# Kernel tuning notes

Measured on AMD Instinct MI355X. Metric: run time of the kernel, lower is better.

## Reference

```python
import jax, jax.numpy as jnp
import numpy as np

B, S, P, N = 256, 128, 100, 500
E, H, L, F = 256, 4, 2, 1024   # embed, heads, layers, ffn
V, U, I = 50000, 10000, 10000


def setup_inputs() -> dict:
    key = jax.random.key(0)
    ks = jax.random.split(key, 32)
    u = lambda k, shp: jax.random.uniform(k, shp, jnp.float32, -0.1, 0.1)
    n = lambda k, shp, s=0.02: jax.random.normal(k, shp, jnp.float32) * s
    inp = {
        'attr': jax.random.randint(ks[0], (B, S), 0, V),
        'attr_inds': jax.random.randint(ks[1], (B, S), 0, S),
        'attr_tf': jax.random.uniform(ks[2], (B, S), jnp.float32),
        'attr_feat': jax.random.normal(ks[3], (B, 13), jnp.float32),
        'attr_lens': jax.random.randint(ks[4], (B,), S // 2, S + 1).at[0].set(S),
        'attr_lens_user': jax.random.randint(ks[5], (B,), 0, S),
        'attr_lens_item': jax.random.randint(ks[6], (B,), 0, S),
        'user_ids': jax.random.randint(ks[7], (B,), 0, U),
        'item_ids': jax.random.randint(ks[8], (B,), 0, I),
        'pos_targets': jax.random.randint(ks[9], (B, P), 0, V),
        'pos_lens': jax.random.randint(ks[10], (B,), 1, P + 1).at[0].set(P),
        'neg_targets': jax.random.randint(ks[11], (B, N), 0, V),
        'neg_lens': jax.random.randint(ks[12], (B,), 1, N + 1).at[0].set(N),
        # parameters (init_uniform(-0.1,0.1) like f_init_weight)
        'attr_emb': u(ks[13], (V, E)),
        'user_emb': u(ks[14], (U, E)),
        'item_emb': u(ks[15], (I, E)),
        'out_emb': u(ks[16], (V, 3 * E)),
        'fw_W': n(ks[17], (1, 13), 0.1),
        'fw_b': jnp.zeros((1,), jnp.float32),
        'qkv_w': n(ks[18], (L, 3 * E, E)),
        'qkv_b': jnp.zeros((L, 3 * E), jnp.float32),
        'attn_out_w': n(ks[19], (L, E, E)),
        'attn_out_b': jnp.zeros((L, E), jnp.float32),
        'ln1_s': jnp.ones((L, E), jnp.float32),
        'ln1_b': jnp.zeros((L, E), jnp.float32),
        'ff1_w': n(ks[20], (L, F, E)),
        'ff1_b': jnp.zeros((L, F), jnp.float32),
        'ff2_w': n(ks[21], (L, E, F)),
        'ff2_b': jnp.zeros((L, E), jnp.float32),
        'ln2_s': jnp.ones((L, E), jnp.float32),
        'ln2_b': jnp.zeros((L, E), jnp.float32),
    }
    return inp


def _ln(x, s, b, eps=1e-5):
    m = jnp.mean(x, axis=-1, keepdims=True)
    v = jnp.mean(jnp.square(x - m), axis=-1, keepdims=True)
    return (x - m) * jax.lax.rsqrt(v + eps) * s + b


def _encoder_layer(x, pad, p):
    # PyTorch TransformerEncoderLayer (post-norm, relu, dropout=0/eval)
    b, s, e = x.shape
    hd = e // H
    qkv = x @ p['qkv_w'].T + p['qkv_b']                      # [B,S,3E]
    q, k, v = jnp.split(qkv, 3, axis=-1)
    q = q.reshape(b, s, H, hd)
    k = k.reshape(b, s, H, hd)
    v = v.reshape(b, s, H, hd)
    scores = jnp.einsum('bqhd,bkhd->bhqk', q, k) / jnp.sqrt(jnp.float32(hd))
    scores = scores + jnp.where(pad[:, None, None, :], -1e9, 0.0)
    a = jax.nn.softmax(scores, axis=-1)
    o = jnp.einsum('bhqk,bkhd->bqhd', a, v).reshape(b, s, e)
    o = o @ p['attn_out_w'].T + p['attn_out_b']
    x = _ln(x + o, p['ln1_s'], p['ln1_b'])
    h = jax.nn.relu(x @ p['ff1_w'].T + p['ff1_b'])
    h = h @ p['ff2_w'].T + p['ff2_b']
    return _ln(x + h, p['ln2_s'], p['ln2_b'])


def reference(attr, attr_inds, attr_tf, attr_feat, attr_lens, attr_lens_user,
              attr_lens_item, user_ids, item_ids, pos_targets, pos_lens,
              neg_targets, neg_lens, attr_emb, user_emb, item_emb, out_emb,
              fw_W, fw_b, qkv_w, qkv_b, attn_out_w, attn_out_b, ln1_s, ln1_b,
              ff1_w, ff1_b, ff2_w, ff2_b, ln2_s, ln2_b):
    b, s = attr.shape
    pos = jnp.arange(s)
    pad = pos[None, :] >= attr_lens[:, None]                 # True = padding
    x = attr_emb[attr]                                       # [B,S,E]
    for l in range(qkv_w.shape[0]):
        p = {'qkv_w': qkv_w[l], 'qkv_b': qkv_b[l],
             'attn_out_w': attn_out_w[l], 'attn_out_b': attn_out_b[l],
             'ln1_s': ln1_s[l], 'ln1_b': ln1_b[l],
             'ff1_w': ff1_w[l], 'ff1_b': ff1_b[l],
             'ff2_w': ff2_w[l], 'ff2_b': ff2_b[l],
             'ln2_s': ln2_s[l], 'ln2_b': ln2_b[l]}
        x = _encoder_layer(x, pad, p)
    # per-sample scalar user weight; vectorized ragged user/item tf weighting
    w_user = jax.nn.sigmoid(attr_feat @ fw_W.T + fw_b)[:, 0]           # [B]
    side = jnp.where(pos[None, :] < attr_lens_user[:, None],
                     w_user[:, None], 1.0 - w_user[:, None])           # [B,S]
    weight = attr_tf * side * (~pad)                                   # [B,S]
    attr_x = jnp.einsum('bs,bse->be', weight, x)                       # [B,E]
    output = jnp.concatenate([user_emb[user_ids], attr_x,
                              item_emb[item_ids]], axis=-1)            # [B,3E]
    pos_logits = jnp.einsum('bpe,be->bp', out_emb[pos_targets], output)
    neg_logits = jnp.einsum('bne,be->bn', out_emb[neg_targets], output)
    pos_valid = jnp.arange(pos_targets.shape[1])[None, :] < pos_lens[:, None]
    neg_valid = jnp.arange(neg_targets.shape[1])[None, :] < neg_lens[:, None]
    logits = jnp.concatenate([pos_logits, neg_logits], axis=-1)
    mask = jnp.concatenate([pos_valid, neg_valid], axis=-1)
    new_targets = jnp.concatenate([jnp.ones_like(pos_targets),
                                   jnp.zeros_like(neg_targets)], axis=1)
    new_targets = new_targets * mask.astype(new_targets.dtype)
    return logits, mask, new_targets
```

## Files before the change

kernel.cpp:

```cpp
#include <hip/hip_runtime.h>
#include <hip/hip_bf16.h>

typedef __bf16 bf16_t;
typedef __bf16 bf16x8 __attribute__((ext_vector_type(8)));
typedef __bf16 bf16x4 __attribute__((ext_vector_type(4)));
typedef float f32x4 __attribute__((ext_vector_type(4)));

#define B_ 256
#define S_ 128
#define E_ 256
#define H_ 4
#define HD_ 64
#define F_ 1024
#define TPOS_ 100
#define TNEG_ 500
#define TT_ 600
#define ROWS_ (B_ * S_)

__global__ __launch_bounds__(256) void cvtall_kernel(
        const float* __restrict__ sq, const float* __restrict__ sa,
        const float* __restrict__ s1, const float* __restrict__ s2,
        bf16_t* __restrict__ dq, bf16_t* __restrict__ da,
        bf16_t* __restrict__ d1, bf16_t* __restrict__ d2) {
    int i = blockIdx.x * 256 + threadIdx.x;
    if (i < 393216) { dq[i] = (bf16_t)sq[i]; }
    else if (i < 524288) { int j = i - 393216; da[j] = (bf16_t)sa[j]; }
    else if (i < 1048576) { int j = i - 524288; d1[j] = (bf16_t)s1[j]; }
    else { int j = i - 1048576; d2[j] = (bf16_t)s2[j]; }
}

__global__ __launch_bounds__(256) void embed_kernel(const int* __restrict__ attr,
        const float* __restrict__ emb, bf16_t* __restrict__ xb) {
    int row = blockIdx.x * 4 + (threadIdx.x >> 6);
    int lane = threadIdx.x & 63;
    int idx = attr[row];
    float4 v = reinterpret_cast<const float4*>(emb + (size_t)idx * E_)[lane];
    bf16x4 o; o[0] = (bf16_t)v.x; o[1] = (bf16_t)v.y; o[2] = (bf16_t)v.z; o[3] = (bf16_t)v.w;
    *reinterpret_cast<bf16x4*>(xb + (size_t)row * E_ + lane * 4) = o;
}

template<bool RELU>
__global__ __launch_bounds__(256) void gemm_kernel(
        const bf16_t* __restrict__ A, const bf16_t* __restrict__ W,
        const float* __restrict__ bias, bf16_t* __restrict__ outB, int M, int N, int K) {
    __shared__ bf16_t lA[2][128 * 32];
    __shared__ bf16_t lB[2][128 * 32];
    int tid = threadIdx.x;
    int wave = tid >> 6, lane = tid & 63;
    int wr = wave >> 1, wc = wave & 1;
    int mBase = blockIdx.y * 128;
    int nBase = blockIdx.x * 128;
    int r16 = lane & 15, kg = lane >> 4;

    int srow = wave * 16 + (lane >> 2);
    int scol = (lane & 3) * 8;
    const bf16_t* gA = A + (size_t)(mBase + srow) * K + scol;
    const bf16_t* gB = W + (size_t)(nBase + srow) * K + scol;
    int ldst = wave * 512;

    f32x4 acc[4][4] = {};

    #define STAGE(buf, k0) { \
        _Pragma("unroll") \
        for (int iss = 0; iss < 2; iss++) { \
            __builtin_amdgcn_global_load_lds( \
                (const __attribute__((address_space(1))) void*)(gA + (size_t)iss * 64 * K + (k0)), \
                (__attribute__((address_space(3))) void*)(&lA[buf][iss * 2048 + ldst]), 16, 0, 0); \
            __builtin_amdgcn_global_load_lds( \
                (const __attribute__((address_space(1))) void*)(gB + (size_t)iss * 64 * K + (k0)), \
                (__attribute__((address_space(3))) void*)(&lB[buf][iss * 2048 + ldst]), 16, 0, 0); \
        } }

    STAGE(0, 0);
    int cur = 0;
    for (int k0 = 0; k0 < K; k0 += 32) {
        __syncthreads();
        if (k0 + 32 < K) STAGE(cur ^ 1, k0 + 32);
        bf16x8 a[4], b[4];
        #pragma unroll
        for (int i = 0; i < 4; i++) {
            a[i] = *reinterpret_cast<const bf16x8*>(&lA[cur][(wr * 64 + i * 16 + r16) * 32 + kg * 8]);
            b[i] = *reinterpret_cast<const bf16x8*>(&lB[cur][(wc * 64 + i * 16 + r16) * 32 + kg * 8]);
        }
        #pragma unroll
        for (int mi = 0; mi < 4; mi++)
            #pragma unroll
            for (int ni = 0; ni < 4; ni++)
                acc[mi][ni] = __builtin_amdgcn_mfma_f32_16x16x32_bf16(a[mi], b[ni], acc[mi][ni], 0, 0, 0);
        cur ^= 1;
    }
    #undef STAGE

    #pragma unroll
    for (int mi = 0; mi < 4; mi++) {
        #pragma unroll
        for (int ni = 0; ni < 4; ni++) {
            int col = nBase + wc * 64 + ni * 16 + r16;
            float bv = bias[col];
            #pragma unroll
            for (int j = 0; j < 4; j++) {
                int row = mBase + wr * 64 + mi * 16 + kg * 4 + j;
                float v = acc[mi][ni][j] + bv;
                if (RELU) v = v > 0.f ? v : 0.f;
                outB[(size_t)row * N + col] = (bf16_t)v;
            }
        }
    }
}

__global__ __launch_bounds__(256) void gemm_ln_kernel(
        const bf16_t* __restrict__ A, const bf16_t* __restrict__ W,
        const float* __restrict__ bias, const float* __restrict__ sc,
        const float* __restrict__ bi, bf16_t* __restrict__ xb, int M, int K) {
    __shared__ bf16_t lA[2][64 * 32];
    __shared__ bf16_t lB[2][256 * 32];
    __shared__ float psum[64][2][2];
    int tid = threadIdx.x;
    int wave = tid >> 6, lane = tid & 63;
    int wm = wave >> 1, wn = wave & 1;
    int mBase = blockIdx.x * 64;
    int r16 = lane & 15, kg = lane >> 4;

    const bf16_t* gA = A + (size_t)(mBase + wave * 16 + (lane >> 2)) * K + (lane & 3) * 8;
    const bf16_t* gB = W + (size_t)((lane >> 2)) * K + (lane & 3) * 8;

    f32x4 acc[2][8] = {};

    #define STAGE2(buf, k0) { \
        __builtin_amdgcn_global_load_lds( \
            (const __attribute__((address_space(1))) void*)(gA + (k0)), \
            (__attribute__((address_space(3))) void*)(&lA[buf][wave * 512]), 16, 0, 0); \
        _Pragma("unroll") \
        for (int iss = 0; iss < 4; iss++) { \
            int q = wave * 4 + iss; \
            __builtin_amdgcn_global_load_lds( \
                (const __attribute__((address_space(1))) void*)(gB + (size_t)q * 16 * K + (k0)), \
                (__attribute__((address_space(3))) void*)(&lB[buf][q * 512]), 16, 0, 0); \
        } }

    STAGE2(0, 0);
    int cur = 0;
    for (int k0 = 0; k0 < K; k0 += 32) {
        __syncthreads();
        if (k0 + 32 < K) STAGE2(cur ^ 1, k0 + 32);
        bf16x8 a[2], b[8];
        #pragma unroll
        for (int mi = 0; mi < 2; mi++)
            a[mi] = *reinterpret_cast<const bf16x8*>(&lA[cur][(wm * 32 + mi * 16 + r16) * 32 + kg * 8]);
        #pragma unroll
        for (int ni = 0; ni < 8; ni++)
            b[ni] = *reinterpret_cast<const bf16x8*>(&lB[cur][(wn * 128 + ni * 16 + r16) * 32 + kg * 8]);
        #pragma unroll
        for (int mi = 0; mi < 2; mi++)
            #pragma unroll
            for (int ni = 0; ni < 8; ni++)
                acc[mi][ni] = __builtin_amdgcn_mfma_f32_16x16x32_bf16(a[mi], b[ni], acc[mi][ni], 0, 0, 0);
        cur ^= 1;
    }
    #undef STAGE2

    float bv[8];
    #pragma unroll
    for (int ni = 0; ni < 8; ni++) bv[ni] = bias[wn * 128 + ni * 16 + r16];
    #pragma unroll
    for (int mi = 0; mi < 2; mi++) {
        #pragma unroll
        for (int j = 0; j < 4; j++) {
            int rl = wm * 32 + mi * 16 + kg * 4 + j;
            const bf16_t* rrow = xb + (size_t)(mBase + rl) * 256;
            float s = 0.f, q = 0.f;
            #pragma unroll
            for (int ni = 0; ni < 8; ni++) {
                int col = wn * 128 + ni * 16 + r16;
                float v = acc[mi][ni][j] + bv[ni] + (float)rrow[col];
                acc[mi][ni][j] = v;
                s += v; q += v * v;
            }
            #pragma unroll
            for (int m = 1; m < 16; m <<= 1) { s += __shfl_xor(s, m); q += __shfl_xor(q, m); }
            if (r16 == 0) { psum[rl][wn][0] = s; psum[rl][wn][1] = q; }
        }
    }
    __syncthreads();
    #pragma unroll
    for (int mi = 0; mi < 2; mi++) {
        #pragma unroll
        for (int j = 0; j < 4; j++) {
            int rl = wm * 32 + mi * 16 + kg * 4 + j;
            float s = psum[rl][0][0] + psum[rl][1][0];
            float qq = psum[rl][0][1] + psum[rl][1][1];
            float mean = s * (1.0f / 256.0f);
            float var = qq * (1.0f / 256.0f) - mean * mean;
            float inv = rsqrtf(var + 1e-5f);
            bf16_t* orow = xb + (size_t)(mBase + rl) * 256;
            #pragma unroll
            for (int ni = 0; ni < 8; ni++) {
                int col = wn * 128 + ni * 16 + r16;
                float o = (acc[mi][ni][j] - mean) * inv * sc[col] + bi[col];
                orow[col] = (bf16_t)o;
            }
        }
    }
}

__global__ __launch_bounds__(256) void attn_kernel(const bf16_t* __restrict__ qkv,
        const int* __restrict__ lens, bf16_t* __restrict__ out) {
    __shared__ bf16_t p[S_][S_ + 8];
    __shared__ bf16_t vl[HD_][S_ + 8];
    int bh = blockIdx.x; int b = bh >> 2, h = bh & 3;
    int wave = threadIdx.x >> 6, lane = threadIdx.x & 63;
    int r16 = lane & 15, kg = lane >> 4;
    int q0 = wave * 32;
    int len = lens[b];
    const bf16_t* qbase = qkv + (size_t)b * S_ * 768;

    {
        int sl = (wave & 1) * 64 + lane;
        const bf16_t* vsrc = qbase + (size_t)sl * 768 + 512 + h * HD_;
        #pragma unroll
        for (int pass = 0; pass < 4; pass++) {
            int d0 = (pass * 2 + (wave >> 1)) * 8;
            bf16x8 v = *reinterpret_cast<const bf16x8*>(vsrc + d0);
            #pragma unroll
            for (int j = 0; j < 8; j++) vl[d0 + j][sl] = v[j];
        }
    }

    f32x4 acc[2][8] = {};
    #pragma unroll
    for (int ks = 0; ks < 2; ks++) {
        int kOff = h * HD_ + ks * 32 + kg * 8;
        bf16x8 a[2], bb[8];
        #pragma unroll
        for (int mi = 0; mi < 2; mi++)
            a[mi] = *reinterpret_cast<const bf16x8*>(qbase + (size_t)(q0 + mi * 16 + r16) * 768 + kOff);
        #pragma unroll
        for (int ni = 0; ni < 8; ni++)
            bb[ni] = *reinterpret_cast<const bf16x8*>(qbase + (size_t)(ni * 16 + r16) * 768 + 256 + kOff);
        #pragma unroll
        for (int mi = 0; mi < 2; mi++)
            #pragma unroll
            for (int ni = 0; ni < 8; ni++)
                acc[mi][ni] = __builtin_amdgcn_mfma_f32_16x16x32_bf16(a[mi], bb[ni], acc[mi][ni], 0, 0, 0);
    }
    #pragma unroll
    for (int mi = 0; mi < 2; mi++) {
        #pragma unroll
        for (int j = 0; j < 4; j++) {
            float vals[8]; float mx = -1e30f;
            #pragma unroll
            for (int ni = 0; ni < 8; ni++) {
                int kp = ni * 16 + r16;
                float v = acc[mi][ni][j] * 0.125f;
                vals[ni] = (kp < len) ? v : -1e30f;
                mx = fmaxf(mx, vals[ni]);
            }
            #pragma unroll
            for (int m = 1; m < 16; m <<= 1) mx = fmaxf(mx, __shfl_xor(mx, m));
            float sum = 0.f;
            #pragma unroll
            for (int ni = 0; ni < 8; ni++) {
                vals[ni] = (vals[ni] > -1e29f) ? __expf(vals[ni] - mx) : 0.f;
                sum += vals[ni];
            }
            #pragma unroll
            for (int m = 1; m < 16; m <<= 1) sum += __shfl_xor(sum, m);
            float inv = 1.0f / sum;
            int row = q0 + mi * 16 + kg * 4 + j;
            #pragma unroll
            for (int ni = 0; ni < 8; ni++)
                p[row][ni * 16 + r16] = (bf16_t)(vals[ni] * inv);
        }
    }
    __syncthreads();
    f32x4 acc2[2][4] = {};
    #pragma unroll
    for (int ks = 0; ks < 4; ks++) {
        int k = ks * 32 + kg * 8;
        bf16x8 a[2], bb[4];
        #pragma unroll
        for (int mi = 0; mi < 2; mi++)
            a[mi] = *reinterpret_cast<const bf16x8*>(&p[q0 + mi * 16 + r16][k]);
        #pragma unroll
        for (int ni = 0; ni < 4; ni++)
            bb[ni] = *reinterpret_cast<const bf16x8*>(&vl[ni * 16 + r16][k]);
        #pragma unroll
        for (int mi = 0; mi < 2; mi++)
            #pragma unroll
            for (int ni = 0; ni < 4; ni++)
                acc2[mi][ni] = __builtin_amdgcn_mfma_f32_16x16x32_bf16(a[mi], bb[ni], acc2[mi][ni], 0, 0, 0);
    }
    #pragma unroll
    for (int mi = 0; mi < 2; mi++)
        #pragma unroll
        for (int ni = 0; ni < 4; ni++)
            #pragma unroll
            for (int j = 0; j < 4; j++) {
                int q = q0 + mi * 16 + kg * 4 + j;
                int d = ni * 16 + r16;
                out[((size_t)b * S_ + q) * E_ + h * HD_ + d] = (bf16_t)acc2[mi][ni][j];
            }
}

__global__ void wuser_kernel(const float* __restrict__ feat, const float* __restrict__ W,
                             const float* __restrict__ bb, float* __restrict__ wu) {
    int b = threadIdx.x;
    if (b < B_) {
        float z = bb[0];
        #pragma unroll
        for (int i = 0; i < 13; i++) z += feat[b * 13 + i] * W[i];
        wu[b] = 1.f / (1.f + __expf(-z));
    }
}

__global__ __launch_bounds__(256) void pool_kernel(
        const bf16_t* __restrict__ xb, const float* __restrict__ attr_tf,
        const int* __restrict__ lens, const int* __restrict__ lens_user,
        const float* __restrict__ wu, const int* __restrict__ uid, const int* __restrict__ iid,
        const float* __restrict__ user_emb, const float* __restrict__ item_emb,
        float* __restrict__ outvec) {
    int b = blockIdx.x, t = threadIdx.x;
    __shared__ float wrow[S_];
    if (t < S_) {
        float w = (t < lens[b]) ? attr_tf[b * S_ + t] : 0.f;
        float side = (t < lens_user[b]) ? wu[b] : (1.f - wu[b]);
        wrow[t] = w * side;
    }
    __syncthreads();
    float acc = 0.f;
    const bf16_t* xr = xb + (size_t)b * S_ * E_ + t;
    #pragma unroll 4
    for (int s = 0; s < S_; s++) acc += wrow[s] * (float)xr[(size_t)s * E_];
    outvec[b * 768 + 256 + t] = acc;
    outvec[b * 768 + t] = user_emb[(size_t)uid[b] * E_ + t];
    outvec[b * 768 + 512 + t] = item_emb[(size_t)iid[b] * E_ + t];
}

__global__ __launch_bounds__(256) void logits_kernel(
        const float* __restrict__ outvec, const float* __restrict__ out_emb,
        const int* __restrict__ pos_t, const int* __restrict__ pos_l,
        const int* __restrict__ neg_t, const int* __restrict__ neg_l,
        float* __restrict__ dout) {
    int g = blockIdx.x * 4 + (threadIdx.x >> 6);
    int lane = threadIdx.x & 63;
    int b = g / TT_, t = g - b * TT_;
    int tgt, valid, ispos;
    if (t < TPOS_) { tgt = pos_t[b * TPOS_ + t]; valid = (t < pos_l[b]); ispos = 1; }
    else { int tn = t - TPOS_; tgt = neg_t[b * TNEG_ + tn]; valid = (tn < neg_l[b]); ispos = 0; }
    const float4* e4 = reinterpret_cast<const float4*>(out_emb + (size_t)tgt * 768);
    const float4* o4 = reinterpret_cast<const float4*>(outvec + (size_t)b * 768);
    float acc = 0.f;
    #pragma unroll
    for (int c = 0; c < 3; c++) {
        float4 a = e4[c * 64 + lane];
        float4 o = o4[c * 64 + lane];
        acc += a.x * o.x + a.y * o.y + a.z * o.z + a.w * o.w;
    }
    #pragma unroll
    for (int m = 1; m < 64; m <<= 1) acc += __shfl_xor(acc, m);
    if (lane == 0) {
        size_t i = (size_t)b * TT_ + t;
        dout[i] = acc;
        dout[(size_t)B_ * TT_ + i] = valid ? 1.0f : 0.0f;
        dout[2 * (size_t)B_ * TT_ + i] = (valid && ispos) ? 1.0f : 0.0f;
    }
}

extern "C" void kernel_launch(void* const* d_in, const int* in_sizes, int n_in,
                              void* d_out, int out_size, void* d_ws, size_t ws_size,
                              hipStream_t stream) {
    const int*   attr        = (const int*)d_in[0];
    const float* attr_tf     = (const float*)d_in[2];
    const float* attr_feat   = (const float*)d_in[3];
    const int*   attr_lens   = (const int*)d_in[4];
    const int*   attr_lens_u = (const int*)d_in[5];
    const int*   user_ids    = (const int*)d_in[7];
    const int*   item_ids    = (const int*)d_in[8];
    const int*   pos_targets = (const int*)d_in[9];
    const int*   pos_lens    = (const int*)d_in[10];
    const int*   neg_targets = (const int*)d_in[11];
    const int*   neg_lens    = (const int*)d_in[12];
    const float* attr_emb    = (const float*)d_in[13];
    const float* user_emb    = (const float*)d_in[14];
    const float* item_emb    = (const float*)d_in[15];
    const float* out_emb     = (const float*)d_in[16];
    const float* fw_W        = (const float*)d_in[17];
    const float* fw_b        = (const float*)d_in[18];
    const float* qkv_w       = (const float*)d_in[19];
    const float* qkv_b       = (const float*)d_in[20];
    const float* attn_out_w  = (const float*)d_in[21];
    const float* attn_out_b  = (const float*)d_in[22];
    const float* ln1_s       = (const float*)d_in[23];
    const float* ln1_b       = (const float*)d_in[24];
    const float* ff1_w       = (const float*)d_in[25];
    const float* ff1_b       = (const float*)d_in[26];
    const float* ff2_w       = (const float*)d_in[27];
    const float* ff2_b       = (const float*)d_in[28];
    const float* ln2_s       = (const float*)d_in[29];
    const float* ln2_b       = (const float*)d_in[30];

    size_t szRes = (size_t)ROWS_ * E_ * 2;
    size_t wB = (size_t)1572864 * 2;
    size_t fixedB = 2 * szRes + wB + (size_t)B_ * 768 * 4 + 4096 + 16384;
    int CH = 32;
    for (int ch = 1; ch <= 32; ch <<= 1) {
        if (fixedB + (size_t)(ROWS_ / ch) * 1024 * 2 <= ws_size) { CH = ch; break; }
    }
    int rowsC = ROWS_ / CH, sampC = B_ / CH;

    char* ws = (char*)d_ws;
    size_t off = 0;
    auto alloc = [&](size_t bytes) { void* pp = ws + off; off += (bytes + 255) & ~255ULL; return pp; };
    bf16_t* xb  = (bf16_t*)alloc(szRes);
    bf16_t* ob  = (bf16_t*)alloc(szRes);
    bf16_t* wq  = (bf16_t*)alloc((size_t)393216 * 2);
    bf16_t* wa  = (bf16_t*)alloc((size_t)131072 * 2);
    bf16_t* w1  = (bf16_t*)alloc((size_t)524288 * 2);
    bf16_t* w2  = (bf16_t*)alloc((size_t)524288 * 2);
    float* outvec = (float*)alloc((size_t)B_ * 768 * 4);
    float* wu     = (float*)alloc(1024);
    bf16_t* chunk = (bf16_t*)alloc((size_t)rowsC * 1024 * 2);

    cvtall_kernel<<<6144, 256, 0, stream>>>(qkv_w, attn_out_w, ff1_w, ff2_w, wq, wa, w1, w2);
    embed_kernel<<<ROWS_ / 4, 256, 0, stream>>>(attr, attr_emb, xb);

    for (int l = 0; l < 2; l++) {
        for (int c = 0; c < CH; c++) {
            size_t r0 = (size_t)c * rowsC;
            gemm_kernel<false><<<dim3(6, rowsC / 128), 256, 0, stream>>>(
                xb + r0 * E_, wq + (size_t)l * 768 * 256, qkv_b + l * 768, chunk, rowsC, 768, 256);
            attn_kernel<<<sampC * H_, 256, 0, stream>>>(chunk, attr_lens + c * sampC, ob + r0 * E_);
        }
        gemm_ln_kernel<<<ROWS_ / 64, 256, 0, stream>>>(
            ob, wa + (size_t)l * 256 * 256, attn_out_b + l * 256,
            ln1_s + l * 256, ln1_b + l * 256, xb, ROWS_, 256);
        for (int c = 0; c < CH; c++) {
            size_t r0 = (size_t)c * rowsC;
            gemm_kernel<true><<<dim3(8, rowsC / 128), 256, 0, stream>>>(
                xb + r0 * E_, w1 + (size_t)l * 1024 * 256, ff1_b + l * 1024, chunk, rowsC, 1024, 256);
            gemm_ln_kernel<<<rowsC / 64, 256, 0, stream>>>(
                chunk, w2 + (size_t)l * 256 * 1024, ff2_b + l * 256,
                ln2_s + l * 256, ln2_b + l * 256, xb + r0 * E_, rowsC, 1024);
        }
    }

    wuser_kernel<<<1, 256, 0, stream>>>(attr_feat, fw_W, fw_b, wu);
    pool_kernel<<<B_, 256, 0, stream>>>(xb, attr_tf, attr_lens, attr_lens_u, wu,
                                        user_ids, item_ids, user_emb, item_emb, outvec);
    logits_kernel<<<B_ * TT_ / 4, 256, 0, stream>>>(outvec, out_emb, pos_targets, pos_lens,
                                                    neg_targets, neg_lens, (float*)d_out);
}
```

Baseline: 389.4 us.

## Replace per-target gathered dot products with dense vocab GEMM then gather

Instead of gathering one 768-float out_emb row per (sample, target) pair and reducing it against the output vector, the code now computes logits for every vocabulary row against all 256 sample vectors with a bf16 MFMA GEMM. The result goes into a workspace buffer, and a light kernel then gathers the needed entries and writes the masks. This streams out_emb once instead of re-reading rows for about 150K targets. In exchange it does extra compute for unused vocab entries, writes a logits buffer of about 51MB, and rounds both the output vector and out_emb to bf16.

```diff
diff --git a/kernel.cpp b/kernel.cpp
--- a/kernel.cpp
+++ b/kernel.cpp
@@ -16,6 +16,8 @@
 #define TNEG_ 500
 #define TT_ 600
 #define ROWS_ (B_ * S_)
+#define V_ 50000
+#define LF_ 50048
 
 __global__ __launch_bounds__(256) void cvtall_kernel(
         const float* __restrict__ sq, const float* __restrict__ sa,
@@ -318,7 +320,7 @@
         const int* __restrict__ lens, const int* __restrict__ lens_user,
         const float* __restrict__ wu, const int* __restrict__ uid, const int* __restrict__ iid,
         const float* __restrict__ user_emb, const float* __restrict__ item_emb,
-        float* __restrict__ outvec) {
+        bf16_t* __restrict__ outvecb) {
     int b = blockIdx.x, t = threadIdx.x;
     __shared__ float wrow[S_];
     if (t < S_) {
@@ -331,39 +333,108 @@
     const bf16_t* xr = xb + (size_t)b * S_ * E_ + t;
     #pragma unroll 4
     for (int s = 0; s < S_; s++) acc += wrow[s] * (float)xr[(size_t)s * E_];
-    outvec[b * 768 + 256 + t] = acc;
-    outvec[b * 768 + t] = user_emb[(size_t)uid[b] * E_ + t];
-    outvec[b * 768 + 512 + t] = item_emb[(size_t)iid[b] * E_ + t];
-}
-
-__global__ __launch_bounds__(256) void logits_kernel(
-        const float* __restrict__ outvec, const float* __restrict__ out_emb,
+    outvecb[b * 768 + 256 + t] = (bf16_t)acc;
+    outvecb[b * 768 + t] = (bf16_t)user_emb[(size_t)uid[b] * E_ + t];
+    outvecb[b * 768 + 512 + t] = (bf16_t)item_emb[(size_t)iid[b] * E_ + t];
+}
+
+__global__ __launch_bounds__(256) void vgemm_kernel(
+        const bf16_t* __restrict__ Ab, const float* __restrict__ oemb,
+        float* __restrict__ lf) {
+    __shared__ bf16_t lA[2][256 * 32];
+    __shared__ bf16_t lB[2][64 * 32];
+    int tid = threadIdx.x;
+    int wave = tid >> 6, lane = tid & 63;
+    int r16 = lane & 15, kg = lane >> 4;
+    int nBase = blockIdx.x * 64;
+
+    int brow = tid >> 2;
+    int bcol = (tid & 3) * 8;
+    int vrow = nBase + brow; if (vrow > V_ - 1) vrow = V_ - 1;
+    const float* gBr = oemb + (size_t)vrow * 768 + bcol;
+
+    int arow = tid >> 2;
+    int acol = (tid & 3) * 8;
+    const bf16_t* gA = Ab + (size_t)arow * 768 + acol;
+
+    #define STAGEA3(buf, k0) { \
+        _Pragma("unroll") \
+        for (int iss = 0; iss < 4; iss++) { \
+            __builtin_amdgcn_global_load_lds( \
+                (const __attribute__((address_space(1))) void*)(gA + (size_t)iss * 64 * 768 + (k0)), \
+                (__attribute__((address_space(3))) void*)(&lA[buf][iss * 2048 + wave * 512]), 16, 0, 0); \
+        } }
+
+    #define LOADB(dst, k0) { \
+        float4 t0 = *reinterpret_cast<const float4*>(gBr + (k0)); \
+        float4 t1 = *reinterpret_cast<const float4*>(gBr + (k0) + 4); \
+        dst[0] = (bf16_t)t0.x; dst[1] = (bf16_t)t0.y; dst[2] = (bf16_t)t0.z; dst[3] = (bf16_t)t0.w; \
+        dst[4] = (bf16_t)t1.x; dst[5] = (bf16_t)t1.y; dst[6] = (bf16_t)t1.z; dst[7] = (bf16_t)t1.w; }
+
+    f32x4 acc[4] = {};
+    f32x4 acc2[4][4] = {};
+
+    bf16x8 bload;
+    STAGEA3(0, 0);
+    LOADB(bload, 0);
+    *reinterpret_cast<bf16x8*>(&lB[0][brow * 32 + bcol]) = bload;
+    LOADB(bload, 32);
+
+    int cur = 0;
+    for (int k0 = 0; k0 < 768; k0 += 32) {
+        __syncthreads();
+        if (k0 + 32 < 768) {
+            STAGEA3(cur ^ 1, k0 + 32);
+            *reinterpret_cast<bf16x8*>(&lB[cur ^ 1][brow * 32 + bcol]) = bload;
+        }
+        if (k0 + 64 < 768) LOADB(bload, k0 + 64);
+        bf16x8 a[4], b[4];
+        #pragma unroll
+        for (int i = 0; i < 4; i++) {
+            a[i] = *reinterpret_cast<const bf16x8*>(&lA[cur][(wave * 64 + i * 16 + r16) * 32 + kg * 8]);
+            b[i] = *reinterpret_cast<const bf16x8*>(&lB[cur][(i * 16 + r16) * 32 + kg * 8]);
+        }
+        #pragma unroll
+        for (int mi = 0; mi < 4; mi++)
+            #pragma unroll
+            for (int ni = 0; ni < 4; ni++)
+                acc2[mi][ni] = __builtin_amdgcn_mfma_f32_16x16x32_bf16(a[mi], b[ni], acc2[mi][ni], 0, 0, 0);
+        cur ^= 1;
+    }
+    #undef STAGEA3
+    #undef LOADB
+
+    #pragma unroll
+    for (int mi = 0; mi < 4; mi++) {
+        #pragma unroll
+        for (int ni = 0; ni < 4; ni++) {
+            int col = nBase + ni * 16 + r16;
+            if (col < V_) {
+                #pragma unroll
+                for (int j = 0; j < 4; j++) {
+                    int row = wave * 64 + mi * 16 + kg * 4 + j;
+                    lf[(size_t)row * LF_ + col] = acc2[mi][ni][j];
+                }
+            }
+        }
+    }
+}
+
+__global__ __launch_bounds__(256) void lgather_kernel(
+        const float* __restrict__ lf,
         const int* __restrict__ pos_t, const int* __restrict__ pos_l,
         const int* __restrict__ neg_t, const int* __restrict__ neg_l,
         float* __restrict__ dout) {
-    int g = blockIdx.x * 4 + (threadIdx.x >> 6);
-    int lane = threadIdx.x & 63;
-    int b = g / TT_, t = g - b * TT_;
+    int i = blockIdx.x * 256 + threadIdx.x;
+    if (i >= B_ * TT_) return;
+    int b = i / TT_, t = i - b * TT_;
     int tgt, valid, ispos;
     if (t < TPOS_) { tgt = pos_t[b * TPOS_ + t]; valid = (t < pos_l[b]); ispos = 1; }
     else { int tn = t - TPOS_; tgt = neg_t[b * TNEG_ + tn]; valid = (tn < neg_l[b]); ispos = 0; }
-    const float4* e4 = reinterpret_cast<const float4*>(out_emb + (size_t)tgt * 768);
-    const float4* o4 = reinterpret_cast<const float4*>(outvec + (size_t)b * 768);
-    float acc = 0.f;
-    #pragma unroll
-    for (int c = 0; c < 3; c++) {
-        float4 a = e4[c * 64 + lane];
-        float4 o = o4[c * 64 + lane];
-        acc += a.x * o.x + a.y * o.y + a.z * o.z + a.w * o.w;
-    }
-    #pragma unroll
-    for (int m = 1; m < 64; m <<= 1) acc += __shfl_xor(acc, m);
-    if (lane == 0) {
-        size_t i = (size_t)b * TT_ + t;
-        dout[i] = acc;
-        dout[(size_t)B_ * TT_ + i] = valid ? 1.0f : 0.0f;
-        dout[2 * (size_t)B_ * TT_ + i] = (valid && ispos) ? 1.0f : 0.0f;
-    }
+    size_t o = (size_t)b * TT_ + t;
+    dout[o] = lf[(size_t)b * LF_ + tgt];
+    dout[(size_t)B_ * TT_ + o] = valid ? 1.0f : 0.0f;
+    dout[2 * (size_t)B_ * TT_ + o] = (valid && ispos) ? 1.0f : 0.0f;
 }
 
 extern "C" void kernel_launch(void* const* d_in, const int* in_sizes, int n_in,
@@ -401,7 +472,8 @@
 
     size_t szRes = (size_t)ROWS_ * E_ * 2;
     size_t wB = (size_t)1572864 * 2;
-    size_t fixedB = 2 * szRes + wB + (size_t)B_ * 768 * 4 + 4096 + 16384;
+    size_t lfB = (size_t)B_ * LF_ * 4;
+    size_t fixedB = 2 * szRes + wB + lfB + (size_t)B_ * 768 * 2 + 4096 + 16384;
     int CH = 32;
     for (int ch = 1; ch <= 32; ch <<= 1) {
         if (fixedB + (size_t)(ROWS_ / ch) * 1024 * 2 <= ws_size) { CH = ch; break; }
@@ -417,7 +489,8 @@
     bf16_t* wa  = (bf16_t*)alloc((size_t)131072 * 2);
     bf16_t* w1  = (bf16_t*)alloc((size_t)524288 * 2);
     bf16_t* w2  = (bf16_t*)alloc((size_t)524288 * 2);
-    float* outvec = (float*)alloc((size_t)B_ * 768 * 4);
+    float* lf    = (float*)alloc(lfB);
+    bf16_t* outvecb = (bf16_t*)alloc((size_t)B_ * 768 * 2);
     float* wu     = (float*)alloc(1024);
     bf16_t* chunk = (bf16_t*)alloc((size_t)rowsC * 1024 * 2);
 
@@ -446,7 +519,8 @@
 
     wuser_kernel<<<1, 256, 0, stream>>>(attr_feat, fw_W, fw_b, wu);
     pool_kernel<<<B_, 256, 0, stream>>>(xb, attr_tf, attr_lens, attr_lens_u, wu,
-                                        user_ids, item_ids, user_emb, item_emb, outvec);
-    logits_kernel<<<B_ * TT_ / 4, 256, 0, stream>>>(outvec, out_emb, pos_targets, pos_lens,
-                                                    neg_targets, neg_lens, (float*)d_out);
-}
+                                        user_ids, item_ids, user_emb, item_emb, outvecb);
+    vgemm_kernel<<<(V_ + 63) / 64, 256, 0, stream>>>(outvecb, out_emb, lf);
+    lgather_kernel<<<(B_ * TT_ + 255) / 256, 256, 0, stream>>>(
+        lf, pos_targets, pos_lens, neg_targets, neg_lens, (float*)d_out);
+}
```

Measured after the change: 413.0 us. +6.1%, slower.
